# Kernel tuning notes

Hardware: AMD Instinct MI355X
Metric: run time of the kernel (lower is better)

Reference implementation:

```python
import jax, jax.numpy as jnp
import numpy as np

EMBED_DIM = 1024
HEADS = 16
HEAD_DIM = EMBED_DIM // HEADS


def setup_inputs() -> dict:
    key = jax.random.key(0)
    ks = jax.random.split(key, 5)
    B, N, C = 2, 2048, EMBED_DIM
    scale = 1.0 / np.sqrt(C)
    x = jax.random.normal(ks[0], (B, N, C), dtype=jnp.float32)
    W_qkv = jax.random.normal(ks[1], (C, 3 * C), dtype=jnp.float32) * scale
    b_qkv = jax.random.normal(ks[2], (3 * C,), dtype=jnp.float32) * 0.01
    W_out = jax.random.normal(ks[3], (C, C), dtype=jnp.float32) * scale
    b_out = jax.random.normal(ks[4], (C,), dtype=jnp.float32) * 0.01
    return {"x": x, "W_qkv": W_qkv, "b_qkv": b_qkv, "W_out": W_out, "b_out": b_out}


def reference(x, W_qkv, b_qkv, W_out, b_out):
    B, N, C = x.shape
    qkv = x @ W_qkv + b_qkv                      # [B, N, 3C]
    qkv = qkv.reshape(B, N, 3, HEADS, HEAD_DIM)
    qkv = jnp.transpose(qkv, (2, 0, 3, 1, 4))    # [3, B, H, N, d]
    q, k, v = qkv[0], qkv[1], qkv[2]
    attn = jnp.einsum('bhnd,bhmd->bhnm', q, k) / np.sqrt(HEAD_DIM)
    attn = jax.nn.softmax(attn, axis=-1)
    out = jnp.einsum('bhnm,bhmd->bhnd', attn, v)  # [B, H, N, d]
    out = jnp.transpose(out, (0, 2, 1, 3)).reshape(B, N, C)
    return out @ W_out + b_out
```

## Files before the change

### kernel.cpp

```cpp
#include <hip/hip_runtime.h>
#include <stdint.h>

typedef __bf16 bf16_t;
typedef bf16_t bf16x8 __attribute__((ext_vector_type(8)));
typedef bf16_t bf16x2v __attribute__((ext_vector_type(2)));
typedef float f32x4 __attribute__((ext_vector_type(4)));
typedef float f32x16 __attribute__((ext_vector_type(16)));
typedef uint32_t u32x2 __attribute__((ext_vector_type(2)));
typedef uint32_t u32x4 __attribute__((ext_vector_type(4)));

#define BATCH 2
#define SEQ 2048
#define CDIM 1024
#define NH 16
#define HD 64

#define QSCALE 0.18033688011f

__device__ __forceinline__ uint16_t f32_bf16(float f) {
    __bf16 h = (__bf16)f;
    return __builtin_bit_cast(uint16_t, h);
}

__device__ __forceinline__ uint32_t pack_bf16(float a, float b) {
    bf16x2v t;
    t.x = (__bf16)a;
    t.y = (__bf16)b;
    return __builtin_bit_cast(uint32_t, t);
}

__device__ __forceinline__ bf16x8 ld8(const uint16_t* p) {
    return *reinterpret_cast<const bf16x8*>(p);
}

__device__ __forceinline__ void swap32(uint32_t& a, uint32_t& b) {
#if __has_builtin(__builtin_amdgcn_permlane32_swap)
    u32x2 r = __builtin_amdgcn_permlane32_swap(a, b, false, false);
    a = r.x;
    b = r.y;
#else
    asm("v_permlane32_swap_b32 %0, %1" : "+v"(a), "+v"(b));
#endif
}

__device__ __forceinline__ void gld16(const uint16_t* g, uint16_t* l) {
    __builtin_amdgcn_global_load_lds(
        (__attribute__((address_space(1))) void*)(g),
        (__attribute__((address_space(3))) void*)(l), 16, 0, 0);
}

#define LDS_FENCE() asm volatile("s_waitcnt lgkmcnt(0)" ::: "memory")
#define WAIT_K_DMA() do { \
    asm volatile("s_waitcnt vmcnt(4)" ::: "memory"); \
    __builtin_amdgcn_sched_barrier(0); \
} while (0)

__global__ __launch_bounds__(256) void prep_kernel(
        const float* __restrict__ x, uint16_t* __restrict__ x_bf,
        const float* __restrict__ Wqkv, uint16_t* __restrict__ wqkvT,
        const float* __restrict__ Wout, uint16_t* __restrict__ woutT) {
    const int bid = blockIdx.x, tid = threadIdx.x;
    if (bid < 4096) {
        int i = (bid * 256 + tid) * 4;
        float4 v = *(const float4*)(x + i);
        ushort4 o;
        o.x = f32_bf16(v.x);
        o.y = f32_bf16(v.y);
        o.z = f32_bf16(v.z);
        o.w = f32_bf16(v.w);
        *(ushort4*)(x_bf + i) = o;
        return;
    }
    __shared__ float tile[32][33];
    const float* in;
    uint16_t* outp;
    int idx, Cc, ncx;
    if (bid < 4096 + 3072) { idx = bid - 4096; in = Wqkv; outp = wqkvT; Cc = 3072; ncx = 96; }
    else                   { idx = bid - 7168; in = Wout; outp = woutT; Cc = 1024; ncx = 32; }
    const int R = 1024;
    int bx = idx % ncx, by = idx / ncx;
    int c0 = bx * 32, r0 = by * 32;
    int tx = tid & 31, ty = tid >> 5;
#pragma unroll
    for (int i = 0; i < 4; i++)
        tile[ty + i * 8][tx] = in[(size_t)(r0 + ty + i * 8) * Cc + c0 + tx];
    __syncthreads();
    const int rr = tid >> 3, seg = tid & 7;
    ushort4 o;
    o.x = f32_bf16(tile[seg * 4 + 0][rr]);
    o.y = f32_bf16(tile[seg * 4 + 1][rr]);
    o.z = f32_bf16(tile[seg * 4 + 2][rr]);
    o.w = f32_bf16(tile[seg * 4 + 3][rr]);
    *(ushort4*)(outp + (size_t)(c0 + rr) * R + r0 + seg * 4) = o;
}

template <int BM, int BN, int MODE>
__global__ __launch_bounds__(256) void gemm_t(
        const uint16_t* __restrict__ A, const uint16_t* __restrict__ Bt, int K,
        const float* __restrict__ bias,
        uint16_t* __restrict__ qw, uint16_t* __restrict__ kw, uint16_t* __restrict__ vt,
        float* __restrict__ out) {
    constexpr int WT_M = BM / 2, WT_N = BN / 2;
    constexpr int MI = WT_M / 16, NJ = WT_N / 16;
    constexpr int ASEG_W = BM / 64, BSEG_W = BN / 64;
    constexpr int AB = 2 * BM * 32 + 2 * BN * 32;
    constexpr int TS = (MODE == 0) ? 4 * 64 * 68 : 0;
    constexpr int SM = AB > TS ? AB : TS;
    __shared__ uint16_t smem[SM];
    uint16_t* As = smem;
    uint16_t* Bs = smem + 2 * BM * 32;

    const int m0 = blockIdx.y * BM, n0 = blockIdx.x * BN;
    const int tid = threadIdx.x;
    const int w = tid >> 6, lane = tid & 63;
    const int quad = lane >> 4, l16 = lane & 15;
    const int wm = (w >> 1) * WT_M, wn = (w & 1) * WT_N;

    const int srow = lane >> 2;
    const int schunk = (lane & 3) ^ (srow & 3);

    const uint16_t* aP[ASEG_W];
    const uint16_t* bP[BSEG_W];
    int aL[ASEG_W], bL[BSEG_W];
#pragma unroll
    for (int s = 0; s < ASEG_W; s++) {
        int seg = w * ASEG_W + s;
        aP[s] = A + (size_t)(m0 + seg * 16 + srow) * K + schunk * 8;
        aL[s] = seg * 512;
    }
#pragma unroll
    for (int s = 0; s < BSEG_W; s++) {
        int seg = w * BSEG_W + s;
        bP[s] = Bt + (size_t)(n0 + seg * 16 + srow) * K + schunk * 8;
        bL[s] = seg * 512;
    }

    auto stage = [&](int buf, int k0) {
#pragma unroll
        for (int s = 0; s < ASEG_W; s++) gld16(aP[s] + k0, As + buf * BM * 32 + aL[s]);
#pragma unroll
        for (int s = 0; s < BSEG_W; s++) gld16(bP[s] + k0, Bs + buf * BN * 32 + bL[s]);
    };

    const int cslot = (quad ^ (l16 & 3)) * 8;
    f32x4 acc[MI][NJ] = {};

    stage(0, 0);
    const int iters = K / 32;
    for (int it = 0; it < iters; ++it) {
        __syncthreads();
        if (it + 1 < iters) stage((it + 1) & 1, (it + 1) * 32);
        const uint16_t* A_ = As + (it & 1) * BM * 32;
        const uint16_t* B_ = Bs + (it & 1) * BN * 32;
        bf16x8 af[MI], bfr[NJ];
#pragma unroll
        for (int i = 0; i < MI; i++) af[i] = ld8(&A_[(wm + i * 16 + l16) * 32 + cslot]);
#pragma unroll
        for (int j = 0; j < NJ; j++) bfr[j] = ld8(&B_[(wn + j * 16 + l16) * 32 + cslot]);
#pragma unroll
        for (int i = 0; i < MI; i++)
#pragma unroll
            for (int j = 0; j < NJ; j++)
                acc[i][j] = __builtin_amdgcn_mfma_f32_16x16x32_bf16(af[i], bfr[j], acc[i][j], 0, 0, 0);
    }

    const int nbase = n0 + wn;
    float bj[NJ];
#pragma unroll
    for (int j = 0; j < NJ; j++) bj[j] = bias[nbase + j * 16 + l16];

    if constexpr (MODE == 1) {
#pragma unroll
        for (int j = 0; j < NJ; j++) {
#pragma unroll
            for (int i = 0; i < MI; i++)
#pragma unroll
                for (int r = 0; r < 4; r++) {
                    int m = m0 + wm + i * 16 + quad * 4 + r;
                    out[(size_t)m * CDIM + nbase + j * 16 + l16] = acc[i][j][r] + bj[j];
                }
        }
    } else {
        __syncthreads();
        uint16_t* T = smem + w * 64 * 68;
        const int gmb = m0 + wm;
        const int b = gmb >> 11, ns0 = gmb & 2047;
        const int lrow = lane >> 3, lch = lane & 7;

        if (nbase < 2048) {
            const int which = nbase >> 10, h = (nbase & 1023) >> 6;
            const float sc = (which == 0) ? QSCALE : 1.0f;
#pragma unroll
            for (int i = 0; i < 4; i++)
#pragma unroll
                for (int j = 0; j < 4; j++)
#pragma unroll
                    for (int r = 0; r < 4; r++)
                        T[(i * 16 + quad * 4 + r) * 68 + j * 16 + l16] =
                            f32_bf16((acc[i][j][r] + bj[j]) * sc);
            LDS_FENCE();
            uint16_t* dst = ((which == 0) ? qw : kw) +
                            (((size_t)b * NH + h) * SEQ + ns0) * HD;
#pragma unroll
            for (int g = 0; g < 8; g++) {
                int r = g * 8 + lrow;
                bf16x8 v = ld8(&T[r * 68 + lch * 8]);
                *(bf16x8*)(dst + (size_t)r * HD + lch * 8) = v;
            }
        } else {
#pragma unroll
            for (int i = 0; i < 4; i++)
#pragma unroll
                for (int j = 0; j < 4; j++) {
                    u32x2 pr;
                    pr.x = pack_bf16(acc[i][j][0] + bj[j], acc[i][j][1] + bj[j]);
                    pr.y = pack_bf16(acc[i][j][2] + bj[j], acc[i][j][3] + bj[j]);
                    *(u32x2*)&T[(j * 16 + l16) * 68 + i * 16 + quad * 4] = pr;
                }
            LDS_FENCE();
            const int h = (nbase - 2048) >> 6;
            uint16_t* dstb = vt + ((size_t)b * NH + h) * HD * SEQ + ns0;
#pragma unroll
            for (int g = 0; g < 8; g++) {
                int dr = g * 8 + lrow;
                bf16x8 v2 = ld8(&T[dr * 68 + lch * 8]);
                *(bf16x8*)(dstb + (size_t)dr * SEQ + lch * 8) = v2;
            }
        }
    }
}

__global__ __launch_bounds__(256) void attn_kernel(
        const uint16_t* __restrict__ qg, const uint16_t* __restrict__ kg,
        const uint16_t* __restrict__ vt, uint16_t* __restrict__ og) {
    __shared__ uint16_t Ks[2][128 * 64];
    __shared__ uint16_t Vs[2][64 * 128];

    const int bh = blockIdx.x;
    const int qt = blockIdx.y;
    const int tid = threadIdx.x;
    const int w = tid >> 6, lane = tid & 63;
    const int l32 = lane & 31, hi = lane >> 5;
    const int qrow0 = qt * 128 + w * 32;
    const size_t base = (size_t)bh * SEQ * HD;

    bf16x8 qf[4];
#pragma unroll
    for (int s = 0; s < 4; s++)
        qf[s] = ld8(qg + base + (size_t)(qrow0 + l32) * HD + s * 16 + hi * 8);

    const int krow = lane >> 3;
    const int kch = (lane & 7) ^ krow;
    const int vrow = lane >> 4;
    const uint16_t* ksrc[4];
    const uint16_t* vsrc[4];
#pragma unroll
    for (int s = 0; s < 4; s++) {
        int seg = w * 4 + s;
        ksrc[s] = kg + base + (size_t)(seg * 8 + krow) * HD + kch * 8;
        int vd = seg * 4 + vrow;
        int vch = (lane & 15) ^ (vd & 15);
        vsrc[s] = vt + base + (size_t)vd * SEQ + vch * 8;
    }

    f32x16 o_acc[2] = {};
    float l_red = 0.0f;

    auto stage = [&](int buf) {
#pragma unroll
        for (int s = 0; s < 4; s++) {
            int seg = w * 4 + s;
            gld16(ksrc[s], &Ks[buf][seg * 512]);
            ksrc[s] += 128 * HD;
        }
#pragma unroll
        for (int s = 0; s < 4; s++) {
            int seg = w * 4 + s;
            gld16(vsrc[s], &Vs[buf][seg * 512]);
            vsrc[s] += 128;
        }
    };

    stage(0);

    const int kxe = l32 & 7;
    const int vxe = l32 & 15;
    const int krowb = l32 * 64;
    const int vrowb = l32 * 128;
    int kco[4];
#pragma unroll
    for (int s = 0; s < 4; s++) kco[s] = ((2 * s + hi) ^ kxe) * 8;
    int vco[4][2];
#pragma unroll
    for (int kvb = 0; kvb < 4; kvb++)
#pragma unroll
        for (int cp = 0; cp < 2; cp++)
            vco[kvb][cp] = ((kvb * 4 + cp * 2 + hi) ^ vxe) * 8;

    const f32x16 fzero = {};
    const int wbase = w * 2048;

    f32x16 S[2];
    WAIT_K_DMA();
    {
        bf16x8 k0[4];
#pragma unroll
        for (int s = 0; s < 4; s++) k0[s] = ld8(&Ks[0][wbase] + krowb + kco[s]);
        S[0] = fzero;
#pragma unroll
        for (int s = 0; s < 4; s++)
            S[0] = __builtin_amdgcn_mfma_f32_32x32x16_bf16(k0[s], qf[s], S[0], 0, 0, 0);
    }

    const int NT = SEQ / 128;
    for (int it = 0; it < NT; ++it) {
        __syncthreads();
        if (it + 1 < NT) stage((it + 1) & 1);
        const uint16_t* K_ = Ks[it & 1];
        const uint16_t* V_ = Vs[it & 1];

#pragma unroll
        for (int ph = 0; ph < 4; ph++) {
            const int cur = ph & 1, nxt = cur ^ 1;
            const int kvb = (w + ph) & 3;
            const bool have_next = (ph < 3) || (it + 1 < NT);

            bf16x8 kf[4];
            if (ph < 3) {
                const int kvbn = (w + ph + 1) & 3;
#pragma unroll
                for (int s = 0; s < 4; s++)
                    kf[s] = ld8(K_ + kvbn * 2048 + krowb + kco[s]);
            } else if (it + 1 < NT) {
                WAIT_K_DMA();
#pragma unroll
                for (int s = 0; s < 4; s++)
                    kf[s] = ld8(&Ks[(it + 1) & 1][wbase] + krowb + kco[s]);
            }

            bf16x8 vf[2][2];
#pragma unroll
            for (int cp = 0; cp < 2; cp++)
#pragma unroll
                for (int mf = 0; mf < 2; mf++)
                    vf[cp][mf] = ld8(V_ + vrowb + mf * 4096 + vco[kvb][cp]);

            float p[16];
#pragma unroll
            for (int i = 0; i < 16; i++) p[i] = __builtin_amdgcn_exp2f(S[cur][i]);
            {
                float s0 = (p[0] + p[1]) + (p[2] + p[3]);
                float s1 = (p[4] + p[5]) + (p[6] + p[7]);
                float s2 = (p[8] + p[9]) + (p[10] + p[11]);
                float s3 = (p[12] + p[13]) + (p[14] + p[15]);
                l_red += (s0 + s1) + (s2 + s3);
            }
            uint32_t pk0[4], pk1[4];
#pragma unroll
            for (int c = 0; c < 4; c++) {
                pk0[c] = pack_bf16(p[4 * c + 0], p[4 * c + 1]);
                pk1[c] = pack_bf16(p[4 * c + 2], p[4 * c + 3]);
            }

            if (have_next) {
                S[nxt] = fzero;
#pragma unroll
                for (int s = 0; s < 4; s++)
                    S[nxt] = __builtin_amdgcn_mfma_f32_32x32x16_bf16(kf[s], qf[s], S[nxt], 0, 0, 0);
            }

#pragma unroll
            for (int cp = 0; cp < 2; cp++) {
                uint32_t b0 = pk0[2 * cp], b2 = pk0[2 * cp + 1];
                uint32_t b1 = pk1[2 * cp], b3 = pk1[2 * cp + 1];
                swap32(b0, b2);
                swap32(b1, b3);
                u32x4 t;
                t.x = b0; t.y = b1; t.z = b2; t.w = b3;
                bf16x8 pb = __builtin_bit_cast(bf16x8, t);
#pragma unroll
                for (int mf = 0; mf < 2; mf++)
                    o_acc[mf] = __builtin_amdgcn_mfma_f32_32x32x16_bf16(vf[cp][mf], pb, o_acc[mf], 0, 0, 0);
            }
        }
    }

    uint32_t la = __builtin_bit_cast(uint32_t, l_red), lb = la;
    swap32(la, lb);
    const float l_tot = __builtin_bit_cast(float, la) + __builtin_bit_cast(float, lb);
    const float inv = __builtin_amdgcn_rcpf(l_tot);

    const int b = bh >> 4, h = bh & 15;
    const int ns = qrow0 + l32;
    uint16_t* orow = og + (((size_t)b * SEQ + ns) * NH + h) * HD;
#pragma unroll
    for (int mf = 0; mf < 2; mf++)
#pragma unroll
        for (int c = 0; c < 4; c++) {
            u32x2 pr;
            pr.x = pack_bf16(o_acc[mf][4 * c + 0] * inv, o_acc[mf][4 * c + 1] * inv);
            pr.y = pack_bf16(o_acc[mf][4 * c + 2] * inv, o_acc[mf][4 * c + 3] * inv);
            *(u32x2*)(orow + mf * 32 + c * 8 + hi * 4) = pr;
        }
}

extern "C" void kernel_launch(void* const* d_in, const int* in_sizes, int n_in,
                              void* d_out, int out_size, void* d_ws, size_t ws_size,
                              hipStream_t stream) {
    const float* x = (const float*)d_in[0];
    const float* Wqkv = (const float*)d_in[1];
    const float* bqkv = (const float*)d_in[2];
    const float* Wout = (const float*)d_in[3];
    const float* bout = (const float*)d_in[4];
    float* out = (float*)d_out;

    uint16_t* ws = (uint16_t*)d_ws;
    uint16_t* x_bf  = ws;
    uint16_t* wqkvT = x_bf + 4194304;
    uint16_t* woutT = wqkvT + 3145728;
    uint16_t* qw    = woutT + 1048576;
    uint16_t* kw    = qw + 4194304;
    uint16_t* vtw   = kw + 4194304;
    uint16_t* attn  = vtw + 4194304;

    prep_kernel<<<8192, 256, 0, stream>>>(x, x_bf, Wqkv, wqkvT, Wout, woutT);

    gemm_t<128, 128, 0><<<dim3(24, 32), 256, 0, stream>>>(
        x_bf, wqkvT, 1024, bqkv, qw, kw, vtw, nullptr);

    attn_kernel<<<dim3(32, 16), 256, 0, stream>>>(qw, kw, vtw, attn);

    gemm_t<64, 128, 1><<<dim3(8, 64), 256, 0, stream>>>(
        attn, woutT, 1024, bout, nullptr, nullptr, nullptr, out);
}
```

Baseline: 178.5 us.

## Process two query tiles per attention block, interleaving their softmax and MFMA

Each attention block now handles 256 query rows instead of 128: every wave keeps two 32-row query fragments, two sets of output accumulators and two row sums. Each K/V tile staged in LDS is therefore reused for twice the queries, which halves K/V global and LDS traffic per query. The exp/pack work of one sub-tile is interleaved with the QK MFMA of the other to hide latency. The grid shrinks from 512 to 256 blocks, and launch_bounds(256,1) allows many more registers per thread, which may lower occupancy and leave some of the 256 CUs idle.

```diff
diff --git a/kernel.cpp b/kernel.cpp
--- a/kernel.cpp
+++ b/kernel.cpp
@@ -230,7 +230,7 @@
     }
 }
 
-__global__ __launch_bounds__(256) void attn_kernel(
+__global__ __launch_bounds__(256, 1) void attn_kernel(
         const uint16_t* __restrict__ qg, const uint16_t* __restrict__ kg,
         const uint16_t* __restrict__ vt, uint16_t* __restrict__ og) {
     __shared__ uint16_t Ks[2][128 * 64];
@@ -241,13 +241,16 @@
     const int tid = threadIdx.x;
     const int w = tid >> 6, lane = tid & 63;
     const int l32 = lane & 31, hi = lane >> 5;
-    const int qrow0 = qt * 128 + w * 32;
+    const int qrow0 = qt * 256 + w * 32;
     const size_t base = (size_t)bh * SEQ * HD;
 
-    bf16x8 qf[4];
-#pragma unroll
-    for (int s = 0; s < 4; s++)
-        qf[s] = ld8(qg + base + (size_t)(qrow0 + l32) * HD + s * 16 + hi * 8);
+    bf16x8 qfA[4], qfB[4];
+#pragma unroll
+    for (int s = 0; s < 4; s++) {
+        const uint16_t* qp = qg + base + (size_t)(qrow0 + l32) * HD + s * 16 + hi * 8;
+        qfA[s] = ld8(qp);
+        qfB[s] = ld8(qp + 128 * HD);
+    }
 
     const int krow = lane >> 3;
     const int kch = (lane & 7) ^ krow;
@@ -263,8 +266,9 @@
         vsrc[s] = vt + base + (size_t)vd * SEQ + vch * 8;
     }
 
-    f32x16 o_acc[2] = {};
-    float l_red = 0.0f;
+    f32x16 o_accA[2] = {};
+    f32x16 o_accB[2] = {};
+    float l_redA = 0.0f, l_redB = 0.0f;
 
     auto stage = [&](int buf) {
 #pragma unroll
@@ -300,16 +304,20 @@
     const f32x16 fzero = {};
     const int wbase = w * 2048;
 
-    f32x16 S[2];
+    f32x16 S_A[2], S_B[2];
     WAIT_K_DMA();
     {
         bf16x8 k0[4];
 #pragma unroll
         for (int s = 0; s < 4; s++) k0[s] = ld8(&Ks[0][wbase] + krowb + kco[s]);
-        S[0] = fzero;
+        S_A[0] = fzero;
+        S_B[0] = fzero;
 #pragma unroll
         for (int s = 0; s < 4; s++)
-            S[0] = __builtin_amdgcn_mfma_f32_32x32x16_bf16(k0[s], qf[s], S[0], 0, 0, 0);
+            S_A[0] = __builtin_amdgcn_mfma_f32_32x32x16_bf16(k0[s], qfA[s], S_A[0], 0, 0, 0);
+#pragma unroll
+        for (int s = 0; s < 4; s++)
+            S_B[0] = __builtin_amdgcn_mfma_f32_32x32x16_bf16(k0[s], qfB[s], S_B[0], 0, 0, 0);
     }
 
     const int NT = SEQ / 128;
@@ -345,34 +353,34 @@
                 for (int mf = 0; mf < 2; mf++)
                     vf[cp][mf] = ld8(V_ + vrowb + mf * 4096 + vco[kvb][cp]);
 
-            float p[16];
-#pragma unroll
-            for (int i = 0; i < 16; i++) p[i] = __builtin_amdgcn_exp2f(S[cur][i]);
+            float pA[16];
+#pragma unroll
+            for (int i = 0; i < 16; i++) pA[i] = __builtin_amdgcn_exp2f(S_A[cur][i]);
             {
-                float s0 = (p[0] + p[1]) + (p[2] + p[3]);
-                float s1 = (p[4] + p[5]) + (p[6] + p[7]);
-                float s2 = (p[8] + p[9]) + (p[10] + p[11]);
-                float s3 = (p[12] + p[13]) + (p[14] + p[15]);
-                l_red += (s0 + s1) + (s2 + s3);
-            }
-            uint32_t pk0[4], pk1[4];
+                float s0 = (pA[0] + pA[1]) + (pA[2] + pA[3]);
+                float s1 = (pA[4] + pA[5]) + (pA[6] + pA[7]);
+                float s2 = (pA[8] + pA[9]) + (pA[10] + pA[11]);
+                float s3 = (pA[12] + pA[13]) + (pA[14] + pA[15]);
+                l_redA += (s0 + s1) + (s2 + s3);
+            }
+            uint32_t a0[4], a1[4];
 #pragma unroll
             for (int c = 0; c < 4; c++) {
-                pk0[c] = pack_bf16(p[4 * c + 0], p[4 * c + 1]);
-                pk1[c] = pack_bf16(p[4 * c + 2], p[4 * c + 3]);
+                a0[c] = pack_bf16(pA[4 * c + 0], pA[4 * c + 1]);
+                a1[c] = pack_bf16(pA[4 * c + 2], pA[4 * c + 3]);
             }
 
             if (have_next) {
-                S[nxt] = fzero;
+                S_B[nxt] = fzero;
 #pragma unroll
                 for (int s = 0; s < 4; s++)
-                    S[nxt] = __builtin_amdgcn_mfma_f32_32x32x16_bf16(kf[s], qf[s], S[nxt], 0, 0, 0);
+                    S_B[nxt] = __builtin_amdgcn_mfma_f32_32x32x16_bf16(kf[s], qfB[s], S_B[nxt], 0, 0, 0);
             }
 
 #pragma unroll
             for (int cp = 0; cp < 2; cp++) {
-                uint32_t b0 = pk0[2 * cp], b2 = pk0[2 * cp + 1];
-                uint32_t b1 = pk1[2 * cp], b3 = pk1[2 * cp + 1];
+                uint32_t b0 = a0[2 * cp], b2 = a0[2 * cp + 1];
+                uint32_t b1 = a1[2 * cp], b3 = a1[2 * cp + 1];
                 swap32(b0, b2);
                 swap32(b1, b3);
                 u32x4 t;
@@ -380,28 +388,84 @@
                 bf16x8 pb = __builtin_bit_cast(bf16x8, t);
 #pragma unroll
                 for (int mf = 0; mf < 2; mf++)
-                    o_acc[mf] = __builtin_amdgcn_mfma_f32_32x32x16_bf16(vf[cp][mf], pb, o_acc[mf], 0, 0, 0);
+                    o_accA[mf] = __builtin_amdgcn_mfma_f32_32x32x16_bf16(vf[cp][mf], pb, o_accA[mf], 0, 0, 0);
+            }
+
+            float pB[16];
+#pragma unroll
+            for (int i = 0; i < 16; i++) pB[i] = __builtin_amdgcn_exp2f(S_B[cur][i]);
+            {
+                float s0 = (pB[0] + pB[1]) + (pB[2] + pB[3]);
+                float s1 = (pB[4] + pB[5]) + (pB[6] + pB[7]);
+                float s2 = (pB[8] + pB[9]) + (pB[10] + pB[11]);
+                float s3 = (pB[12] + pB[13]) + (pB[14] + pB[15]);
+                l_redB += (s0 + s1) + (s2 + s3);
+            }
+            uint32_t c0[4], c1[4];
+#pragma unroll
+            for (int c = 0; c < 4; c++) {
+                c0[c] = pack_bf16(pB[4 * c + 0], pB[4 * c + 1]);
+                c1[c] = pack_bf16(pB[4 * c + 2], pB[4 * c + 3]);
+            }
+
+            if (have_next) {
+                S_A[nxt] = fzero;
+#pragma unroll
+                for (int s = 0; s < 4; s++)
+                    S_A[nxt] = __builtin_amdgcn_mfma_f32_32x32x16_bf16(kf[s], qfA[s], S_A[nxt], 0, 0, 0);
+            }
+
+#pragma unroll
+            for (int cp = 0; cp < 2; cp++) {
+                uint32_t b0 = c0[2 * cp], b2 = c0[2 * cp + 1];
+                uint32_t b1 = c1[2 * cp], b3 = c1[2 * cp + 1];
+                swap32(b0, b2);
+                swap32(b1, b3);
+                u32x4 t;
+                t.x = b0; t.y = b1; t.z = b2; t.w = b3;
+                bf16x8 pb = __builtin_bit_cast(bf16x8, t);
+#pragma unroll
+                for (int mf = 0; mf < 2; mf++)
+                    o_accB[mf] = __builtin_amdgcn_mfma_f32_32x32x16_bf16(vf[cp][mf], pb, o_accB[mf], 0, 0, 0);
             }
         }
     }
 
-    uint32_t la = __builtin_bit_cast(uint32_t, l_red), lb = la;
-    swap32(la, lb);
-    const float l_tot = __builtin_bit_cast(float, la) + __builtin_bit_cast(float, lb);
-    const float inv = __builtin_amdgcn_rcpf(l_tot);
-
     const int b = bh >> 4, h = bh & 15;
-    const int ns = qrow0 + l32;
-    uint16_t* orow = og + (((size_t)b * SEQ + ns) * NH + h) * HD;
-#pragma unroll
-    for (int mf = 0; mf < 2; mf++)
-#pragma unroll
-        for (int c = 0; c < 4; c++) {
-            u32x2 pr;
-            pr.x = pack_bf16(o_acc[mf][4 * c + 0] * inv, o_acc[mf][4 * c + 1] * inv);
-            pr.y = pack_bf16(o_acc[mf][4 * c + 2] * inv, o_acc[mf][4 * c + 3] * inv);
-            *(u32x2*)(orow + mf * 32 + c * 8 + hi * 4) = pr;
-        }
+    {
+        uint32_t la = __builtin_bit_cast(uint32_t, l_redA), lb = la;
+        swap32(la, lb);
+        const float inv = __builtin_amdgcn_rcpf(
+            __builtin_bit_cast(float, la) + __builtin_bit_cast(float, lb));
+        const int ns = qrow0 + l32;
+        uint16_t* orow = og + (((size_t)b * SEQ + ns) * NH + h) * HD;
+#pragma unroll
+        for (int mf = 0; mf < 2; mf++)
+#pragma unroll
+            for (int c = 0; c < 4; c++) {
+                u32x2 pr;
+                pr.x = pack_bf16(o_accA[mf][4 * c + 0] * inv, o_accA[mf][4 * c + 1] * inv);
+                pr.y = pack_bf16(o_accA[mf][4 * c + 2] * inv, o_accA[mf][4 * c + 3] * inv);
+                *(u32x2*)(orow + mf * 32 + c * 8 + hi * 4) = pr;
+            }
+    }
+    {
+        uint32_t la = __builtin_bit_cast(uint32_t, l_redB), lb = la;
+        swap32(la, lb);
+        const float inv = __builtin_amdgcn_rcpf(
+            __builtin_bit_cast(float, la) + __builtin_bit_cast(float, lb));
+        const int ns = qrow0 + 128 + l32;
+        uint16_t* orow = og + (((size_t)b * SEQ + ns) * NH + h) * HD;
+#pragma unroll
+        for (int mf = 0; mf < 2; mf++)
+#pragma unroll
+            for (int c = 0; c < 4; c++) {
+                u32x2 pr;
+                pr.x = pack_bf16(o_accB[mf][4 * c + 0] * inv, o_accB[mf][4 * c + 1] * inv);
+                pr.y = pack_bf16(o_accB[mf][4 * c + 2] * inv, o_accB[mf][4 * c + 3] * inv);
+                *(u32x2*)(orow + mf * 32 + c * 8 + hi * 4) = pr;
+            }
+    }
 }
 
 extern "C" void kernel_launch(void* const* d_in, const int* in_sizes, int n_in,
@@ -428,7 +492,7 @@
     gemm_t<128, 128, 0><<<dim3(24, 32), 256, 0, stream>>>(
         x_bf, wqkvT, 1024, bqkv, qw, kw, vtw, nullptr);
 
-    attn_kernel<<<dim3(32, 16), 256, 0, stream>>>(qw, kw, vtw, attn);
+    attn_kernel<<<dim3(32, 8), 256, 0, stream>>>(qw, kw, vtw, attn);
 
     gemm_t<64, 128, 1><<<dim3(8, 64), 256, 0, stream>>>(
         attn, woutT, 1024, bout, nullptr, nullptr, nullptr, out);
```

New measurement: 180.7 us. No clear change (+1.2%).

## Single-buffer V tile in LDS and preload V fragments to registers

Applied to the files above, without the earlier changes.

The V shared-memory tile drops from double to single buffering, so LDS per block shrinks from 64KB to 48KB. To keep this safe, each iteration loads all V fragments for the tile into registers up front, waits, barriers, and only then issues the next V prefetch. The launch bound is raised to request 3 blocks per CU. The cost is more VGPRs for the 16 preloaded V fragments, an extra barrier per iteration, and a shorter window for the V DMA to overlap compute.

```diff
diff --git a/kernel.cpp b/kernel.cpp
--- a/kernel.cpp
+++ b/kernel.cpp
@@ -230,11 +230,11 @@
     }
 }
 
-__global__ __launch_bounds__(256) void attn_kernel(
+__global__ __launch_bounds__(256, 3) void attn_kernel(
         const uint16_t* __restrict__ qg, const uint16_t* __restrict__ kg,
         const uint16_t* __restrict__ vt, uint16_t* __restrict__ og) {
     __shared__ uint16_t Ks[2][128 * 64];
-    __shared__ uint16_t Vs[2][64 * 128];
+    __shared__ uint16_t Vs[64 * 128];
 
     const int bh = blockIdx.x;
     const int qt = blockIdx.y;
@@ -266,22 +266,25 @@
     f32x16 o_acc[2] = {};
     float l_red = 0.0f;
 
-    auto stage = [&](int buf) {
+    auto stageK = [&](int buf) {
 #pragma unroll
         for (int s = 0; s < 4; s++) {
             int seg = w * 4 + s;
             gld16(ksrc[s], &Ks[buf][seg * 512]);
             ksrc[s] += 128 * HD;
         }
+    };
+    auto stageV = [&]() {
 #pragma unroll
         for (int s = 0; s < 4; s++) {
             int seg = w * 4 + s;
-            gld16(vsrc[s], &Vs[buf][seg * 512]);
+            gld16(vsrc[s], &Vs[seg * 512]);
             vsrc[s] += 128;
         }
     };
 
-    stage(0);
+    stageK(0);
+    stageV();
 
     const int kxe = l32 & 7;
     const int vxe = l32 & 15;
@@ -290,12 +293,6 @@
     int kco[4];
 #pragma unroll
     for (int s = 0; s < 4; s++) kco[s] = ((2 * s + hi) ^ kxe) * 8;
-    int vco[4][2];
-#pragma unroll
-    for (int kvb = 0; kvb < 4; kvb++)
-#pragma unroll
-        for (int cp = 0; cp < 2; cp++)
-            vco[kvb][cp] = ((kvb * 4 + cp * 2 + hi) ^ vxe) * 8;
 
     const f32x16 fzero = {};
     const int wbase = w * 2048;
@@ -315,14 +312,29 @@
     const int NT = SEQ / 128;
     for (int it = 0; it < NT; ++it) {
         __syncthreads();
-        if (it + 1 < NT) stage((it + 1) & 1);
+        if (it + 1 < NT) stageK((it + 1) & 1);
         const uint16_t* K_ = Ks[it & 1];
-        const uint16_t* V_ = Vs[it & 1];
+
+        bf16x8 vfr[4][2][2];
+#pragma unroll
+        for (int ph = 0; ph < 4; ph++) {
+            const int kvb = (w + ph) & 3;
+#pragma unroll
+            for (int cp = 0; cp < 2; cp++)
+#pragma unroll
+                for (int mf = 0; mf < 2; mf++)
+                    vfr[ph][cp][mf] =
+                        ld8(Vs + vrowb + mf * 4096 + (((kvb * 4 + cp * 2 + hi) ^ vxe) * 8));
+        }
+        asm volatile("s_waitcnt lgkmcnt(0)" ::: "memory");
+        __builtin_amdgcn_sched_barrier(0);
+        __builtin_amdgcn_s_barrier();
+        __builtin_amdgcn_sched_barrier(0);
+        if (it + 1 < NT) stageV();
 
 #pragma unroll
         for (int ph = 0; ph < 4; ph++) {
             const int cur = ph & 1, nxt = cur ^ 1;
-            const int kvb = (w + ph) & 3;
             const bool have_next = (ph < 3) || (it + 1 < NT);
 
             bf16x8 kf[4];
@@ -337,13 +349,6 @@
                 for (int s = 0; s < 4; s++)
                     kf[s] = ld8(&Ks[(it + 1) & 1][wbase] + krowb + kco[s]);
             }
-
-            bf16x8 vf[2][2];
-#pragma unroll
-            for (int cp = 0; cp < 2; cp++)
-#pragma unroll
-                for (int mf = 0; mf < 2; mf++)
-                    vf[cp][mf] = ld8(V_ + vrowb + mf * 4096 + vco[kvb][cp]);
 
             float p[16];
 #pragma unroll
@@ -380,7 +385,7 @@
                 bf16x8 pb = __builtin_bit_cast(bf16x8, t);
 #pragma unroll
                 for (int mf = 0; mf < 2; mf++)
-                    o_acc[mf] = __builtin_amdgcn_mfma_f32_32x32x16_bf16(vf[cp][mf], pb, o_acc[mf], 0, 0, 0);
+                    o_acc[mf] = __builtin_amdgcn_mfma_f32_32x32x16_bf16(vfr[ph][cp][mf], pb, o_acc[mf], 0, 0, 0);
             }
         }
     }
```

New measurement: 224.0 us. +25.5%, slower.
